# Kernel optimization log

Measured on AMD Instinct MI355X. Metric: run time of the kernel, lower is better.

The kernel has to match this reference:

```python
import jax, jax.numpy as jnp
import numpy as np

B, GH, GW, DIM, NH = 1, 48, 64, 1536, 16
HD = DIM // NH          # 96
C = HD // 2             # 48, divisible by 3 as the rope split requires
L = max(GH, GW)


def setup_inputs() -> dict:
    key = jax.random.key(0)
    ks = jax.random.split(key, 6)
    x = jax.random.normal(ks[0], (B, GH * GW, DIM), jnp.float32)
    w_init = lambda k: jax.random.normal(k, (DIM, DIM), jnp.float32) * 0.02
    # rope frequency table: theta[p, j] = p / 10000^(j/C); freqs = exp(i*theta)
    pos = jnp.arange(L, dtype=jnp.float32)[:, None]
    inv = 10000.0 ** (-jnp.arange(C, dtype=jnp.float32) / C)
    theta = pos * inv[None, :]
    return {
        "x": x,
        "wq": w_init(ks[1]), "bq": jnp.zeros((DIM,), jnp.float32),
        "wk": w_init(ks[2]), "bk": jnp.zeros((DIM,), jnp.float32),
        "wv": w_init(ks[3]), "bv": jnp.zeros((DIM,), jnp.float32),
        "wo": w_init(ks[4]), "bo": jnp.zeros((DIM,), jnp.float32),
        "freqs_cos": jnp.cos(theta), "freqs_sin": jnp.sin(theta),
        "h": GH, "w": GW,
    }


def rope_apply_spatial(x, freqs_cos, freqs_sin, h, w):
    # x: [b, s, n, d] with s == h*w. Complex rotation done in real arithmetic.
    b, s, n, d = x.shape
    c = d // 2
    c3 = c // 3
    # channel groups: [0:c3] identity (ones), [c3:2c3] rotated by h-position,
    # [2c3:3c3] rotated by w-position  (matches freqs.split + cat in torch)
    cos_hw = jnp.concatenate([
        jnp.ones((h, w, c3), x.dtype),
        jnp.broadcast_to(freqs_cos[:h, None, c3:2 * c3], (h, w, c3)),
        jnp.broadcast_to(freqs_cos[None, :w, 2 * c3:3 * c3], (h, w, c3)),
    ], axis=-1).reshape(1, s, 1, c)
    sin_hw = jnp.concatenate([
        jnp.zeros((h, w, c3), x.dtype),
        jnp.broadcast_to(freqs_sin[:h, None, c3:2 * c3], (h, w, c3)),
        jnp.broadcast_to(freqs_sin[None, :w, 2 * c3:3 * c3], (h, w, c3)),
    ], axis=-1).reshape(1, s, 1, c)
    xc = x.reshape(b, s, n, c, 2)
    xr, xi = xc[..., 0], xc[..., 1]
    yr = xr * cos_hw - xi * sin_hw
    yi = xr * sin_hw + xi * cos_hw
    return jnp.stack([yr, yi], axis=-1).reshape(b, s, n, d)


def reference(x, wq, bq, wk, bk, wv, bv, wo, bo, freqs_cos, freqs_sin, h, w):
    b, s, _ = x.shape
    q = (x @ wq + bq).reshape(b, s, NH, HD)
    k = (x @ wk + bk).reshape(b, s, NH, HD)
    v = (x @ wv + bv).reshape(b, s, NH, HD)
    q = rope_apply_spatial(q, freqs_cos, freqs_sin, h, w)
    k = rope_apply_spatial(k, freqs_cos, freqs_sin, h, w)
    scale = 1.0 / jnp.sqrt(jnp.asarray(HD, q.dtype))
    scores = jnp.einsum('bqnd,bknd->bnqk', q, k) * scale  # [b, n, s, s]
    attn = jax.nn.softmax(scores, axis=-1)
    out = jnp.einsum('bnqk,bknd->bqnd', attn, v).reshape(b, s, NH * HD)
    return out @ wo + bo
```

## Files before the change

### kernel.cpp

```cpp
#include <hip/hip_runtime.h>
#include <math.h>

#define S_LEN 3072
#define DIM 1536
#define NHEADS 16
#define HDIM 96
#define NPAIR 48

typedef __attribute__((ext_vector_type(8))) _Float16 half8;
typedef __attribute__((ext_vector_type(4))) _Float16 half4v;
typedef __attribute__((ext_vector_type(2))) _Float16 half2v;
typedef __attribute__((ext_vector_type(4))) float f32x4;

__device__ inline void gload16(const void* g, void* l) {
    __builtin_amdgcn_global_load_lds(
        (const __attribute__((address_space(1))) void*)g,
        (__attribute__((address_space(3))) void*)l, 16, 0, 0);
}

__device__ inline unsigned int packh2(float a, float b) {
    _Float16 ha = (_Float16)a, hb = (_Float16)b;
    unsigned short ua = *(unsigned short*)&ha;
    unsigned short ub = *(unsigned short*)&hb;
    return (unsigned int)ua | ((unsigned int)ub << 16);
}

__global__ __launch_bounds__(256)
void convert_f32_f16(const float* __restrict__ src, _Float16* __restrict__ dst, int n4)
{
    int i = blockIdx.x * 256 + threadIdx.x;
    if (i < n4) {
        float4 v = *(const float4*)&src[(size_t)i * 4];
        half4v h = { (_Float16)v.x, (_Float16)v.y, (_Float16)v.z, (_Float16)v.w };
        *(half4v*)&dst[(size_t)i * 4] = h;
    }
}

__global__ __launch_bounds__(256)
void transpose_w(const float* __restrict__ w0, const float* __restrict__ w1,
                 const float* __restrict__ w2, const float* __restrict__ w3,
                 _Float16* __restrict__ wt)
{
    __shared__ _Float16 t[64][68];
    const int z = blockIdx.z;
    const float* W = (z == 0) ? w0 : (z == 1) ? w1 : (z == 2) ? w2 : w3;
    _Float16* O = wt + (size_t)z * DIM * DIM;
    const int k0 = blockIdx.y * 64, n0 = blockIdx.x * 64;
    const int tid = threadIdx.x;
    const int r = tid >> 4, c4 = (tid & 15) * 4;
#pragma unroll
    for (int g = 0; g < 4; g++) {
        int kk = r + g * 16;
        float4 v = *(const float4*)&W[(size_t)(k0 + kk) * DIM + n0 + c4];
        t[c4 + 0][kk] = (_Float16)v.x; t[c4 + 1][kk] = (_Float16)v.y;
        t[c4 + 2][kk] = (_Float16)v.z; t[c4 + 3][kk] = (_Float16)v.w;
    }
    __syncthreads();
    const int nr = tid >> 2, ks = (tid & 3) * 16;
#pragma unroll
    for (int s = 0; s < 4; s++)
        *(ushort4*)&O[(size_t)(n0 + nr) * DIM + k0 + ks + s * 4] =
            *(ushort4*)&t[nr][ks + s * 4];
}

template<bool QKV>
__global__ __launch_bounds__(256)
void gemm_f16(const _Float16* __restrict__ X,
              const _Float16* __restrict__ W0t, const _Float16* __restrict__ W1t,
              const _Float16* __restrict__ W2t,
              const float* __restrict__ B0, const float* __restrict__ B1,
              const float* __restrict__ B2,
              void* __restrict__ outv)
{
    __shared__ __align__(16) _Float16 As[128][64];
    __shared__ __align__(16) _Float16 Bs[128][64];

    const int tid = threadIdx.x;
    const int w = tid >> 6, lane = tid & 63;
    const int ln = lane & 15, quad = lane >> 4;
    const int bz = blockIdx.z;
    const _Float16* Wt = W0t; const float* bias = B0;
    if (QKV) { if (bz == 1) { Wt = W1t; bias = B1; } else if (bz == 2) { Wt = W2t; bias = B2; } }
    const int m0 = blockIdx.y * 128, n0 = blockIdx.x * 128;
    const int wm = w >> 1, wn = w & 1;
    const int row8 = lane >> 3, cch = lane & 7;
    const int gch = cch ^ row8;

    f32x4 acc[4][4];
#pragma unroll
    for (int i = 0; i < 4; i++)
#pragma unroll
        for (int j = 0; j < 4; j++) acc[i][j] = (f32x4){0.f, 0.f, 0.f, 0.f};

    for (int k0 = 0; k0 < DIM; k0 += 64) {
        __syncthreads();
#pragma unroll
        for (int j = 0; j < 4; j++) {
            const int r = w * 32 + j * 8;
            gload16(X  + (size_t)(m0 + r + row8) * DIM + k0 + gch * 8, &As[r][0]);
            gload16(Wt + (size_t)(n0 + r + row8) * DIM + k0 + gch * 8, &Bs[r][0]);
        }
        __syncthreads();

        half8 a[4][2], b[4][2];
#pragma unroll
        for (int mt = 0; mt < 4; mt++) {
            int m = wm * 64 + mt * 16 + ln;
#pragma unroll
            for (int ks = 0; ks < 2; ks++) {
                int s = (ks * 4 + quad) ^ (ln & 7);
                a[mt][ks] = *(const half8*)&As[m][s * 8];
            }
        }
#pragma unroll
        for (int nt = 0; nt < 4; nt++) {
            int n = wn * 64 + nt * 16 + ln;
#pragma unroll
            for (int ks = 0; ks < 2; ks++) {
                int s = (ks * 4 + quad) ^ (ln & 7);
                b[nt][ks] = *(const half8*)&Bs[n][s * 8];
            }
        }
#pragma unroll
        for (int ks = 0; ks < 2; ks++)
#pragma unroll
            for (int mt = 0; mt < 4; mt++)
#pragma unroll
                for (int nt = 0; nt < 4; nt++)
                    acc[mt][nt] = __builtin_amdgcn_mfma_f32_16x16x32_f16(
                        a[mt][ks], b[nt][ks], acc[mt][nt], 0, 0, 0);
    }

#pragma unroll
    for (int nt = 0; nt < 4; nt++) {
        int col = n0 + wn * 64 + nt * 16 + ln;
        float bv = bias[col];
        int head = col / HDIM, hd = col % HDIM;
#pragma unroll
        for (int mt = 0; mt < 4; mt++) {
            int row0 = m0 + wm * 64 + mt * 16 + quad * 4;
            if (QKV && bz == 2) {
                half4v p;
#pragma unroll
                for (int r = 0; r < 4; r++) p[r] = (_Float16)(acc[mt][nt][r] + bv);
                *(half4v*)&((_Float16*)outv)[(((size_t)2 * NHEADS + head) * HDIM + hd) * S_LEN + row0] = p;
            } else {
#pragma unroll
                for (int r = 0; r < 4; r++) {
                    float v = acc[mt][nt][r] + bv;
                    if (QKV) {
                        ((_Float16*)outv)[(((size_t)bz * NHEADS + head) * S_LEN + row0 + r) * HDIM + hd]
                            = (_Float16)v;
                    } else {
                        ((float*)outv)[(size_t)(row0 + r) * DIM + col] = v;
                    }
                }
            }
        }
    }
}

__global__ __launch_bounds__(256)
void rope_kernel(_Float16* __restrict__ qh, _Float16* __restrict__ kh,
                 const float* __restrict__ fc, const float* __restrict__ fs)
{
    const int per_tensor = NHEADS * S_LEN * 32;
    int idx = blockIdx.x * 256 + threadIdx.x;
    if (idx >= 2 * per_tensor) return;
    _Float16* buf = (idx < per_tensor) ? qh : kh;
    int r  = idx % per_tensor;
    int head = r / (S_LEN * 32);
    int r2 = r % (S_LEN * 32);
    int s  = r2 >> 5;
    int jc = 16 + (r2 & 31);
    int pos = (jc < 32) ? (s >> 6) : (s & 63);
    float c  = fc[pos * NPAIR + jc];
    float sn = fs[pos * NPAIR + jc];
    size_t base = (((size_t)head * S_LEN) + s) * HDIM + 2 * jc;
    half2v xv = *(half2v*)&buf[base];
    float xr = (float)xv[0], xi = (float)xv[1];
    half2v y = { (_Float16)(xr * c - xi * sn), (_Float16)(xr * sn + xi * c) };
    *(half2v*)&buf[base] = y;
}

__global__ __launch_bounds__(256)
void attn_mfma_kernel(const _Float16* __restrict__ qh, const _Float16* __restrict__ kh,
                      const _Float16* __restrict__ vtg, _Float16* __restrict__ aoh)
{
    __shared__ __align__(16) _Float16 Ks[64][100];
    __shared__ __align__(16) _Float16 Vt[96][68];
    __shared__ __align__(16) _Float16 Pl[4][16][72];

    const int tid  = threadIdx.x;
    const int wid  = tid >> 6;
    const int lane = tid & 63;
    const int ln   = lane & 15;
    const int quad = lane >> 4;
    const int h    = blockIdx.y;
    const int q0   = blockIdx.x * 64;
    const float scale_ = 0.10206207261596577f;

    half8 aq[3];
    {
        const _Float16* qrow = qh + (((size_t)h * S_LEN) + q0 + wid * 16 + ln) * HDIM;
#pragma unroll
        for (int kb3 = 0; kb3 < 3; kb3++) {
            half8 a = *(const half8*)&qrow[kb3 * 32 + quad * 8];
            half8 v;
#pragma unroll
            for (int i = 0; i < 8; i++) v[i] = (_Float16)((float)a[i] * scale_);
            aq[kb3] = v;
        }
    }

    f32x4 o[6];
#pragma unroll
    for (int dn = 0; dn < 6; dn++) o[dn] = (f32x4){0.f, 0.f, 0.f, 0.f};
    float m_ = -INFINITY, l_ = 0.f;

    const _Float16* kbase = kh + ((size_t)h * S_LEN) * HDIM;
    const _Float16* vbase = vtg + ((size_t)h * HDIM) * S_LEN;

    const int krow = tid / 4, kc8 = (tid & 3) * 3;
    const int vrow = tid / 2, vc8 = (tid & 1) * 4;

    for (int kt = 0; kt < S_LEN / 64; ++kt) {
        const int j0 = kt * 64;
        __syncthreads();
#pragma unroll
        for (int u = 0; u < 3; u++) {
            *(uint4*)&Ks[krow][(kc8 + u) * 8] =
                *(const uint4*)&kbase[(size_t)(j0 + krow) * HDIM + (kc8 + u) * 8];
        }
        for (int i = tid; i < 768; i += 256) {
            int d = i >> 3, c = i & 7;
            *(uint4*)&Vt[d][c * 8] =
                *(const uint4*)&vbase[(size_t)d * S_LEN + j0 + c * 8];
        }
        __syncthreads();

        f32x4 s[4];
#pragma unroll
        for (int nb = 0; nb < 4; nb++) {
            f32x4 acc = (f32x4){0.f, 0.f, 0.f, 0.f};
#pragma unroll
            for (int kb3 = 0; kb3 < 3; kb3++) {
                half8 ak = *(const half8*)&Ks[nb * 16 + ln][kb3 * 32 + quad * 8];
                acc = __builtin_amdgcn_mfma_f32_16x16x32_f16(ak, aq[kb3], acc, 0, 0, 0);
            }
            s[nb] = acc;
        }

        float mx = s[0][0];
#pragma unroll
        for (int nb = 0; nb < 4; nb++)
#pragma unroll
            for (int r = 0; r < 4; r++) mx = fmaxf(mx, s[nb][r]);
        mx = fmaxf(mx, __shfl_xor(mx, 16));
        mx = fmaxf(mx, __shfl_xor(mx, 32));
        float mn = fmaxf(m_, mx);
        float al = __expf(m_ - mn);
        m_ = mn;
        float rs = 0.f;
#pragma unroll
        for (int nb = 0; nb < 4; nb++)
#pragma unroll
            for (int r = 0; r < 4; r++) {
                float p = __expf(s[nb][r] - mn);
                s[nb][r] = p;
                rs += p;
            }
        rs += __shfl_xor(rs, 16);
        rs += __shfl_xor(rs, 32);
        l_ = l_ * al + rs;

#pragma unroll
        for (int nb = 0; nb < 4; nb++) {
            uint2 u;
            u.x = packh2(s[nb][0], s[nb][1]);
            u.y = packh2(s[nb][2], s[nb][3]);
            *(uint2*)&Pl[wid][ln][nb * 16 + quad * 4] = u;
        }

#pragma unroll
        for (int dn = 0; dn < 6; dn++)
#pragma unroll
            for (int r = 0; r < 4; r++) o[dn][r] *= al;

        half8 ap[2];
#pragma unroll
        for (int c = 0; c < 2; c++)
            ap[c] = *(const half8*)&Pl[wid][ln][c * 32 + quad * 8];
#pragma unroll
        for (int dn = 0; dn < 6; dn++) {
#pragma unroll
            for (int c = 0; c < 2; c++) {
                half8 av = *(const half8*)&Vt[dn * 16 + ln][c * 32 + quad * 8];
                o[dn] = __builtin_amdgcn_mfma_f32_16x16x32_f16(av, ap[c], o[dn], 0, 0, 0);
            }
        }
    }

    const float invl = 1.f / l_;
    const size_t rowbase = (size_t)(q0 + wid * 16 + ln) * DIM + h * HDIM;
#pragma unroll
    for (int dn = 0; dn < 6; dn++) {
        half4v p;
#pragma unroll
        for (int r = 0; r < 4; r++) p[r] = (_Float16)(o[dn][r] * invl);
        *(half4v*)&aoh[rowbase + dn * 16 + quad * 4] = p;
    }
}

extern "C" void kernel_launch(void* const* d_in, const int* in_sizes, int n_in,
                              void* d_out, int out_size, void* d_ws, size_t ws_size,
                              hipStream_t stream) {
    const float* x  = (const float*)d_in[0];
    const float* wq = (const float*)d_in[1];
    const float* bq = (const float*)d_in[2];
    const float* wk = (const float*)d_in[3];
    const float* bk = (const float*)d_in[4];
    const float* wv = (const float*)d_in[5];
    const float* bv = (const float*)d_in[6];
    const float* wo = (const float*)d_in[7];
    const float* bo = (const float*)d_in[8];
    const float* fc = (const float*)d_in[9];
    const float* fs = (const float*)d_in[10];
    float* out = (float*)d_out;

    const size_t per  = (size_t)NHEADS * S_LEN * HDIM;
    const size_t dim2 = (size_t)DIM * DIM;
    _Float16* hws  = (_Float16*)d_ws;
    _Float16* qkvh = hws;
    _Float16* qh   = qkvh;
    _Float16* kh   = qkvh + per;
    _Float16* vth  = qkvh + 2 * per;
    _Float16* xh   = hws + 3 * per;
    _Float16* wth  = hws + 4 * per;

    convert_f32_f16<<<(int)((S_LEN * DIM / 4 + 255) / 256), 256, 0, stream>>>(
        x, xh, S_LEN * DIM / 4);
    transpose_w<<<dim3(DIM / 64, DIM / 64, 4), 256, 0, stream>>>(wq, wk, wv, wo, wth);

    gemm_f16<true><<<dim3(DIM / 128, S_LEN / 128, 3), 256, 0, stream>>>(
        xh, wth, wth + dim2, wth + 2 * dim2, bq, bk, bv, qkvh);
    rope_kernel<<<(2 * NHEADS * S_LEN * 32) / 256, 256, 0, stream>>>(qh, kh, fc, fs);
    attn_mfma_kernel<<<dim3(S_LEN / 64, NHEADS), 256, 0, stream>>>(qh, kh, vth, xh);
    gemm_f16<false><<<dim3(DIM / 128, S_LEN / 128, 1), 256, 0, stream>>>(
        xh, wth + 3 * dim2, nullptr, nullptr, bo, nullptr, nullptr, out);
}
```

Before: 361.1 us.

## Fuse rope into QKV GEMM epilogue and register-prefetch K/V tiles in attention

Removes the standalone rope kernel and applies the rotation inside the QKV GEMM epilogue, exchanging real/imag partners with a lane shuffle and reading the cos/sin tables directly. This eliminates a kernel launch and a read-modify-write pass over Q and K. Separately, the attention kernel now loads the next K/V tile into registers while computing on the current tile. This overlaps global latency with MFMA work at the cost of extra registers.

```diff
diff --git a/kernel.cpp b/kernel.cpp
--- a/kernel.cpp
+++ b/kernel.cpp
@@ -70,6 +70,7 @@
               const _Float16* __restrict__ W2t,
               const float* __restrict__ B0, const float* __restrict__ B1,
               const float* __restrict__ B2,
+              const float* __restrict__ fc, const float* __restrict__ fs,
               void* __restrict__ outv)
 {
     __shared__ __align__(16) _Float16 As[128][64];
@@ -136,6 +137,8 @@
         int col = n0 + wn * 64 + nt * 16 + ln;
         float bv = bias[col];
         int head = col / HDIM, hd = col % HDIM;
+        int jc = hd >> 1;
+        bool isreal = (ln & 1) == 0;
 #pragma unroll
         for (int mt = 0; mt < 4; mt++) {
             int row0 = m0 + wm * 64 + mt * 16 + quad * 4;
@@ -144,43 +147,32 @@
 #pragma unroll
                 for (int r = 0; r < 4; r++) p[r] = (_Float16)(acc[mt][nt][r] + bv);
                 *(half4v*)&((_Float16*)outv)[(((size_t)2 * NHEADS + head) * HDIM + hd) * S_LEN + row0] = p;
+            } else if (QKV) {
+                float v[4], vp[4];
+#pragma unroll
+                for (int r = 0; r < 4; r++) v[r] = acc[mt][nt][r] + bv;
+#pragma unroll
+                for (int r = 0; r < 4; r++) vp[r] = __shfl_xor(v[r], 1);
+#pragma unroll
+                for (int r = 0; r < 4; r++) {
+                    int srow = row0 + r;
+                    int pos = (jc < 32) ? (srow >> 6) : (srow & 63);
+                    float c  = fc[pos * NPAIR + jc];
+                    float sn = fs[pos * NPAIR + jc];
+                    float xr = isreal ? v[r] : vp[r];
+                    float xi = isreal ? vp[r] : v[r];
+                    float rot = isreal ? (xr * c - xi * sn) : (xr * sn + xi * c);
+                    float outval = (jc < 16) ? v[r] : rot;
+                    ((_Float16*)outv)[(((size_t)bz * NHEADS + head) * S_LEN + srow) * HDIM + hd]
+                        = (_Float16)outval;
+                }
             } else {
 #pragma unroll
-                for (int r = 0; r < 4; r++) {
-                    float v = acc[mt][nt][r] + bv;
-                    if (QKV) {
-                        ((_Float16*)outv)[(((size_t)bz * NHEADS + head) * S_LEN + row0 + r) * HDIM + hd]
-                            = (_Float16)v;
-                    } else {
-                        ((float*)outv)[(size_t)(row0 + r) * DIM + col] = v;
-                    }
-                }
-            }
-        }
-    }
-}
-
-__global__ __launch_bounds__(256)
-void rope_kernel(_Float16* __restrict__ qh, _Float16* __restrict__ kh,
-                 const float* __restrict__ fc, const float* __restrict__ fs)
-{
-    const int per_tensor = NHEADS * S_LEN * 32;
-    int idx = blockIdx.x * 256 + threadIdx.x;
-    if (idx >= 2 * per_tensor) return;
-    _Float16* buf = (idx < per_tensor) ? qh : kh;
-    int r  = idx % per_tensor;
-    int head = r / (S_LEN * 32);
-    int r2 = r % (S_LEN * 32);
-    int s  = r2 >> 5;
-    int jc = 16 + (r2 & 31);
-    int pos = (jc < 32) ? (s >> 6) : (s & 63);
-    float c  = fc[pos * NPAIR + jc];
-    float sn = fs[pos * NPAIR + jc];
-    size_t base = (((size_t)head * S_LEN) + s) * HDIM + 2 * jc;
-    half2v xv = *(half2v*)&buf[base];
-    float xr = (float)xv[0], xi = (float)xv[1];
-    half2v y = { (_Float16)(xr * c - xi * sn), (_Float16)(xr * sn + xi * c) };
-    *(half2v*)&buf[base] = y;
+                for (int r = 0; r < 4; r++)
+                    ((float*)outv)[(size_t)(row0 + r) * DIM + col] = acc[mt][nt][r] + bv;
+            }
+        }
+    }
 }
 
 __global__ __launch_bounds__(256)
@@ -221,23 +213,41 @@
     const _Float16* kbase = kh + ((size_t)h * S_LEN) * HDIM;
     const _Float16* vbase = vtg + ((size_t)h * HDIM) * S_LEN;
 
-    const int krow = tid / 4, kc8 = (tid & 3) * 3;
-    const int vrow = tid / 2, vc8 = (tid & 1) * 4;
+    const int krow = tid >> 2, kc8 = (tid & 3) * 3;
+
+    uint4 kr[3], vr[3];
+#pragma unroll
+    for (int u = 0; u < 3; u++)
+        kr[u] = *(const uint4*)&kbase[(size_t)krow * HDIM + (kc8 + u) * 8];
+#pragma unroll
+    for (int u = 0; u < 3; u++) {
+        int i = tid + u * 256, d = i >> 3, c = i & 7;
+        vr[u] = *(const uint4*)&vbase[(size_t)d * S_LEN + c * 8];
+    }
 
     for (int kt = 0; kt < S_LEN / 64; ++kt) {
-        const int j0 = kt * 64;
         __syncthreads();
 #pragma unroll
+        for (int u = 0; u < 3; u++)
+            *(uint4*)&Ks[krow][(kc8 + u) * 8] = kr[u];
+#pragma unroll
         for (int u = 0; u < 3; u++) {
-            *(uint4*)&Ks[krow][(kc8 + u) * 8] =
-                *(const uint4*)&kbase[(size_t)(j0 + krow) * HDIM + (kc8 + u) * 8];
-        }
-        for (int i = tid; i < 768; i += 256) {
-            int d = i >> 3, c = i & 7;
-            *(uint4*)&Vt[d][c * 8] =
-                *(const uint4*)&vbase[(size_t)d * S_LEN + j0 + c * 8];
+            int i = tid + u * 256, d = i >> 3, c = i & 7;
+            *(uint4*)&Vt[d][c * 8] = vr[u];
         }
         __syncthreads();
+
+        if (kt + 1 < S_LEN / 64) {
+            const int j1 = (kt + 1) * 64;
+#pragma unroll
+            for (int u = 0; u < 3; u++)
+                kr[u] = *(const uint4*)&kbase[(size_t)(j1 + krow) * HDIM + (kc8 + u) * 8];
+#pragma unroll
+            for (int u = 0; u < 3; u++) {
+                int i = tid + u * 256, d = i >> 3, c = i & 7;
+                vr[u] = *(const uint4*)&vbase[(size_t)d * S_LEN + j1 + c * 8];
+            }
+        }
 
         f32x4 s[4];
 #pragma unroll
@@ -343,9 +353,8 @@
     transpose_w<<<dim3(DIM / 64, DIM / 64, 4), 256, 0, stream>>>(wq, wk, wv, wo, wth);
 
     gemm_f16<true><<<dim3(DIM / 128, S_LEN / 128, 3), 256, 0, stream>>>(
-        xh, wth, wth + dim2, wth + 2 * dim2, bq, bk, bv, qkvh);
-    rope_kernel<<<(2 * NHEADS * S_LEN * 32) / 256, 256, 0, stream>>>(qh, kh, fc, fs);
+        xh, wth, wth + dim2, wth + 2 * dim2, bq, bk, bv, fc, fs, qkvh);
     attn_mfma_kernel<<<dim3(S_LEN / 64, NHEADS), 256, 0, stream>>>(qh, kh, vth, xh);
     gemm_f16<false><<<dim3(DIM / 128, S_LEN / 128, 1), 256, 0, stream>>>(
-        xh, wth + 3 * dim2, nullptr, nullptr, bo, nullptr, nullptr, out);
-}
+        xh, wth + 3 * dim2, nullptr, nullptr, bo, nullptr, nullptr, fc, fs, out);
+}
```

After: 474.6 us. 31.4% more time.
